# Kernel tuning notes

Measured on AMD Instinct MI355X. Metric: run time of the kernel, lower is better.

## Reference

```python
import jax, jax.numpy as jnp
import numpy as np

EPS = 1e-6
K = 20
B, N = 4, 4096
HID, CDIM = 128, 64


def vn_lin(W, x):
    # W: [Cout, Cin], x: [B, Cin, 3, ...] -> [B, Cout, 3, ...]
    return jnp.einsum('oc,bc...->bo...', W, x)


def vn_leaky(x, d, ns=0.0):
    # vector-neuron leaky ReLU: reflect the part of x anti-aligned with direction d
    dot = jnp.sum(x * d, axis=2, keepdims=True)
    dsq = jnp.sum(d * d, axis=2, keepdims=True)
    return ns * x + (1.0 - ns) * jnp.where(dot >= 0, x, x - (dot / (dsq + EPS)) * d)


def vn_max_pool(x, Wd):
    # pool over the LAST axis, picking per-(b,c) the vector maximizing <x, d>
    d = vn_lin(Wd, x)
    dot = jnp.sum(x * d, axis=2, keepdims=True)            # [B,C,1,...,L]
    idx = jnp.broadcast_to(jnp.argmax(dot, axis=-1), x.shape[:-1])
    return jnp.take_along_axis(x, idx[..., None], axis=-1)[..., 0]


def graph_feature_cross(pts, k):
    # pts: [B, N, 3] -> [B, 3ch, 3vec, N, k] with channels (nbr-x, x, cross(nbr,x))
    sq = jnp.sum(pts * pts, axis=-1)
    inner = jnp.einsum('bnd,bmd->bnm', pts, pts)
    neg_dist = 2.0 * inner - sq[:, :, None] - sq[:, None, :]
    _, idx = jax.lax.top_k(neg_dist, k)                     # [B, N, k]
    nbr = jax.vmap(lambda p, i: p[i])(pts, idx)             # [B, N, k, 3]
    x = jnp.broadcast_to(pts[:, :, None, :], nbr.shape)
    cross = jnp.cross(nbr, x, axis=-1)
    feat = jnp.stack([nbr - x, x, cross], axis=3)           # [B, N, k, 3ch, 3vec]
    return jnp.transpose(feat, (0, 3, 4, 1, 2))


def resblock(x, a0, f0, a1, f1, sc):
    net = vn_lin(f0, vn_leaky(x, vn_lin(a0, x)))
    dx = vn_lin(f1, vn_leaky(net, vn_lin(a1, net)))
    return vn_lin(sc, x) + dx


def _init(key, shape, fan_in):
    return jax.random.normal(key, shape, jnp.float32) / np.sqrt(fan_in)


def setup_inputs():
    key = jax.random.key(0)
    ks = jax.random.split(key, 14)
    return {
        'pc': jax.random.normal(ks[0], (B, N, 3), jnp.float32),
        'conv_Wf': _init(ks[1], (64, 3), 3),
        'conv_Wd': _init(ks[2], (64, 3), 3),
        'pool_pos_Wd': _init(ks[3], (64, 64), 64),
        'fc_pos_W': _init(ks[4], (2 * HID, 64), 64),
        'blk_a0': _init(ks[5], (5, 2 * HID, 2 * HID), 2 * HID),
        'blk_f0': _init(ks[6], (5, HID, 2 * HID), 2 * HID),
        'blk_a1': _init(ks[7], (5, HID, HID), HID),
        'blk_f1': _init(ks[8], (5, HID, HID), HID),
        'blk_sc': _init(ks[9], (5, HID, 2 * HID), 2 * HID),
        'pool_Wd': _init(ks[10], (5, HID, HID), HID),
        'actc_Wd': _init(ks[11], (HID, HID), HID),
        'fcc_W': _init(ks[12], (CDIM, HID), HID),
    }


def reference(pc, conv_Wf, conv_Wd, pool_pos_Wd, fc_pos_W, blk_a0, blk_f0, blk_a1, blk_f1, blk_sc, pool_Wd, actc_Wd, fcc_W):
    b = pc.shape[0]
    feat = graph_feature_cross(pc, K)                         # [B,3,3,N,k]
    net = vn_leaky(vn_lin(conv_Wf, feat), vn_lin(conv_Wd, feat))  # [B,64,3,N,k]
    net = vn_max_pool(net, pool_pos_Wd)                       # [B,64,3,N] (pool over k)
    net = vn_lin(fc_pos_W, net)                               # [B,256,3,N]
    for i in range(5):
        net = resblock(net, blk_a0[i], blk_f0[i], blk_a1[i], blk_f1[i], blk_sc[i])  # [B,128,3,N]
        if i < 4:
            pooled = vn_max_pool(net, pool_Wd[i])             # [B,128,3] (pool over N)
            net = jnp.concatenate([net, jnp.broadcast_to(pooled[..., None], net.shape)], axis=1)
    net = vn_max_pool(net, pool_Wd[4])                        # [B,128,3]
    c = vn_lin(fcc_W, vn_leaky(net, vn_lin(actc_Wd, net)))    # [B,64,3]
    return c.reshape(b, -1)                                   # [B,192]
```

## Files before the change

kernel.cpp:

```cpp
#include <hip/hip_runtime.h>
#include <hip/hip_bf16.h>
#include <math.h>

#define NPTS 4096
#define NB 4
#define KNN 20
#define NCOLS (3*NPTS)
#define NEG_INF (-__builtin_huge_valf())
#define DNEG_INF (-__builtin_huge_val())

typedef _Float16 f16x8 __attribute__((ext_vector_type(8)));
typedef _Float16 f16x4 __attribute__((ext_vector_type(4)));
typedef float f32x4 __attribute__((ext_vector_type(4)));

#define WOFF_FC 0
#define WOFF_A0 16384
#define WOFF_F0 344064
#define WOFF_A1 507904
#define WOFF_F1 589824
#define WOFF_SC 671744
#define WOFF_PW 835584
#define WTOT    917504

__global__ __launch_bounds__(512) void knn_kernel(const float* __restrict__ pc,
                                                  int* __restrict__ idx) {
  __shared__ float pts[NPTS*3];
  __shared__ double msv[2][8];
  __shared__ int    msn[2][8];
  int b = blockIdx.x >> 10;
  int rowblk = blockIdx.x & 1023;
  const float* pb = pc + (size_t)b*NPTS*3;
  for (int i = threadIdx.x; i < NPTS*3; i += 512) pts[i] = pb[i];
  __syncthreads();
  int wave = threadIdx.x >> 6;
  int lane = threadIdx.x & 63;
  int row  = wave >> 1;
  int half = wave & 1;
  int l128 = half*64 + lane;
  int n = rowblk*4 + row;
  double pn0 = pts[n*3+0], pn1 = pts[n*3+1], pn2 = pts[n*3+2];
  double sqn = pn0*pn0 + pn1*pn1 + pn2*pn2;
  double nd[32];
#pragma unroll
  for (int j = 0; j < 32; ++j) {
    int m = j*128 + l128;
    double q0 = pts[m*3+0], q1 = pts[m*3+1], q2 = pts[m*3+2];
    double inner = pn0*q0 + pn1*q1 + pn2*q2;
    double sqm = q0*q0 + q1*q1 + q2*q2;
    nd[j] = 2.0*inner - sqn - sqm;
  }
  double gm[2]; int gj[2];
#pragma unroll
  for (int g = 0; g < 2; ++g) {
    double v = nd[g*16]; int jb = g*16;
#pragma unroll
    for (int jj = 1; jj < 16; ++jj) {
      int j = g*16 + jj;
      bool take = nd[j] > v;
      v = take ? nd[j] : v;
      jb = take ? j : jb;
    }
    gm[g] = v; gj[g] = jb;
  }
  int* orow = idx + ((size_t)b*NPTS + n)*KNN;
  for (int t = 0; t < KNN; ++t) {
    double bv = gm[0]; int bj = gj[0];
    if (gm[1] > bv) { bv = gm[1]; bj = gj[1]; }
    int bm = bj*128 + l128;
#pragma unroll
    for (int s = 1; s < 64; s <<= 1) {
      double ov = __shfl_xor(bv, s, 64);
      int om = __shfl_xor(bm, s, 64);
      bool take = (ov > bv) || (ov == bv && om < bm);
      bv = take ? ov : bv;
      bm = take ? om : bm;
    }
    if (lane == 0) { msv[t&1][wave] = bv; msn[t&1][wave] = bm; }
    __syncthreads();
    {
      double pv = msv[t&1][wave^1]; int pm = msn[t&1][wave^1];
      bool take = (pv > bv) || (pv == bv && pm < bm);
      bv = take ? pv : bv;
      bm = take ? pm : bm;
    }
    if (half == 0 && lane == 0) orow[t] = bm;
    if (t < KNN-1) {
      int vic_l128 = bm & 127;
      int jw = bm >> 7;
      int vic_half = vic_l128 >> 6;
      if (vic_half == half) {
        bool iswl = (l128 == vic_l128);
        int gw = jw >> 4;
#define REBUILD(G) { \
  _Pragma("unroll") \
  for (int jj = 0; jj < 16; ++jj) { \
    int j = (G)*16 + jj; \
    if (iswl && j == jw) nd[j] = DNEG_INF; \
  } \
  double v = nd[(G)*16]; int jb = (G)*16; \
  _Pragma("unroll") \
  for (int jj = 1; jj < 16; ++jj) { \
    int j = (G)*16 + jj; \
    bool take = nd[j] > v; \
    v = take ? nd[j] : v; \
    jb = take ? j : jb; \
  } \
  gm[G] = v; gj[G] = jb; \
}
        if (gw == 0) REBUILD(0)
        else         REBUILD(1)
#undef REBUILD
      }
    }
  }
}

#define ECH 5
__global__ __launch_bounds__(128) void edgeconv_kernel(
    const float* __restrict__ pc, const int* __restrict__ knnidx,
    const float* __restrict__ Wf, const float* __restrict__ Wd,
    const float* __restrict__ Wp, float* __restrict__ outp) {
  __shared__ float xls[2*ECH*3*64];
  int wave = threadIdx.x >> 6, lane = threadIdx.x & 63;
  int pid0 = blockIdx.x * 2;
  int b = pid0 >> 12;
  int n = (pid0 & (NPTS-1)) + wave;
  const float* pb = pc + (size_t)b*NPTS*3;
  int c = lane;
  float wrow[64];
#pragma unroll
  for (int j = 0; j < 64; ++j) wrow[j] = Wp[c*64 + j];
  float wf0 = Wf[c*3+0], wf1 = Wf[c*3+1], wf2 = Wf[c*3+2];
  float wd0 = Wd[c*3+0], wd1 = Wd[c*3+1], wd2 = Wd[c*3+2];
  float f9[9];
#pragma unroll
  for (int i = 0; i < 9; ++i) f9[i] = 0.0f;
  if (lane < KNN) {
    int j = knnidx[((size_t)b*NPTS + n)*KNN + lane];
    float q0 = pb[j*3+0], q1 = pb[j*3+1], q2 = pb[j*3+2];
    float x0 = pb[n*3+0], x1 = pb[n*3+1], x2 = pb[n*3+2];
    f9[0] = q0-x0; f9[1] = q1-x1; f9[2] = q2-x2;
    f9[3] = x0;    f9[4] = x1;    f9[5] = x2;
    f9[6] = q1*x2 - q2*x1;
    f9[7] = q2*x0 - q0*x2;
    f9[8] = q0*x1 - q1*x0;
  }
  float* xw = &xls[wave*ECH*3*64];
  double bdot = DNEG_INF;
  float bx0 = 0.f, bx1 = 0.f, bx2 = 0.f;
  for (int k0 = 0; k0 < KNN; k0 += ECH) {
    for (int kc = 0; kc < ECH; ++kc) {
      int kk = k0 + kc;
      float fch[9];
#pragma unroll
      for (int i = 0; i < 9; ++i) fch[i] = __shfl(f9[i], kk, 64);
      float fv[3], dv[3];
#pragma unroll
      for (int v = 0; v < 3; ++v) {
        fv[v] = wf0*fch[v] + wf1*fch[3+v] + wf2*fch[6+v];
        dv[v] = wd0*fch[v] + wd1*fch[3+v] + wd2*fch[6+v];
      }
      float dot = fv[0]*dv[0] + fv[1]*dv[1] + fv[2]*dv[2];
      if (dot < 0.0f) {
        float dsq = dv[0]*dv[0] + dv[1]*dv[1] + dv[2]*dv[2];
        float s = dot / (dsq + 1e-6f);
        fv[0] -= s*dv[0]; fv[1] -= s*dv[1]; fv[2] -= s*dv[2];
      }
      xw[(0*ECH+kc)*64 + c] = fv[0];
      xw[(1*ECH+kc)*64 + c] = fv[1];
      xw[(2*ECH+kc)*64 + c] = fv[2];
    }
    for (int kc = 0; kc < ECH; ++kc) {
      float a0 = 0.f, a1 = 0.f, a2 = 0.f;
#pragma unroll
      for (int j = 0; j < 64; j += 4) {
        float4 v0 = *(const float4*)&xw[(0*ECH+kc)*64 + j];
        float4 v1 = *(const float4*)&xw[(1*ECH+kc)*64 + j];
        float4 v2 = *(const float4*)&xw[(2*ECH+kc)*64 + j];
        a0 += wrow[j]*v0.x + wrow[j+1]*v0.y + wrow[j+2]*v0.z + wrow[j+3]*v0.w;
        a1 += wrow[j]*v1.x + wrow[j+1]*v1.y + wrow[j+2]*v1.z + wrow[j+3]*v1.w;
        a2 += wrow[j]*v2.x + wrow[j+1]*v2.y + wrow[j+2]*v2.z + wrow[j+3]*v2.w;
      }
      float xc0 = xw[(0*ECH+kc)*64 + c];
      float xc1 = xw[(1*ECH+kc)*64 + c];
      float xc2 = xw[(2*ECH+kc)*64 + c];
      double dd = (double)xc0*a0 + (double)xc1*a1 + (double)xc2*a2;
      bool take = dd > bdot;
      bdot = take ? dd : bdot;
      bx0 = take ? xc0 : bx0;
      bx1 = take ? xc1 : bx1;
      bx2 = take ? xc2 : bx2;
    }
  }
  outp[((size_t)b*NCOLS + 0*NPTS + n)*64 + c] = bx0;
  outp[((size_t)b*NCOLS + 1*NPTS + n)*64 + c] = bx1;
  outp[((size_t)b*NCOLS + 2*NPTS + n)*64 + c] = bx2;
}

__global__ __launch_bounds__(256) void wsplit_kernel(
    const float* __restrict__ fc, const float* __restrict__ a0,
    const float* __restrict__ f0, const float* __restrict__ a1,
    const float* __restrict__ f1, const float* __restrict__ sc,
    const float* __restrict__ pw, _Float16* __restrict__ outp) {
  int i = blockIdx.x*256 + threadIdx.x;
  const float* src; int off;
  if      (i < WOFF_A0) { src = fc; off = WOFF_FC; }
  else if (i < WOFF_F0) { src = a0; off = WOFF_A0; }
  else if (i < WOFF_A1) { src = f0; off = WOFF_F0; }
  else if (i < WOFF_F1) { src = a1; off = WOFF_A1; }
  else if (i < WOFF_SC) { src = f1; off = WOFF_F1; }
  else if (i < WOFF_PW) { src = sc; off = WOFF_SC; }
  else                  { src = pw; off = WOFF_PW; }
  float w = src[i - off];
  _Float16 h = (_Float16)w;
  outp[i] = h;
  outp[i + WTOT] = (_Float16)(w - (float)h);
}

__global__ __launch_bounds__(256) void bias2_kernel(
    const float* __restrict__ Wa0, const float* __restrict__ Wsc,
    const float* __restrict__ pooled,
    float* __restrict__ biasA, float* __restrict__ biasS) {
  int id = blockIdx.x*256 + threadIdx.x;
  const float* W; float* dst; int Cout; int idx;
  if (id < NB*3*256) { W = Wa0; dst = biasA; Cout = 256; idx = id; }
  else               { W = Wsc; dst = biasS; Cout = 128; idx = id - NB*3*256; }
  int co = idx % Cout; int t = idx / Cout;
  int v = t % 3; int b = t / 3;
  double acc = 0.0;
  const float* wr = W + (size_t)co*256 + 128;
  const float* pp = pooled + (size_t)b*384 + v;
#pragma unroll 4
  for (int c = 0; c < 128; ++c)
    acc += (double)wr[c] * (double)pp[c*3];
  dst[idx] = (float)acc;
}

#define LDP 40
__global__ __launch_bounds__(256) void gemm_mfma(
    const _Float16* __restrict__ Wh, const _Float16* __restrict__ Wl,
    const float* __restrict__ X, const float* __restrict__ Z,
    const float* __restrict__ bias, float* __restrict__ Y,
    int Cin, int Wstride, int ldX, int ldY, int ldZ, int addZ, int Cbias) {
  __shared__ __align__(16) _Float16 Ah[64*LDP];
  __shared__ __align__(16) _Float16 Al[64*LDP];
  __shared__ __align__(16) _Float16 Bh[128*LDP];
  __shared__ __align__(16) _Float16 Bl[128*LDP];
  int b = blockIdx.z;
  int sp0 = blockIdx.x * 64;
  int co0 = blockIdx.y * 128;
  const float* Xb = X + ((size_t)b*NCOLS + sp0) * ldX;
  int t = threadIdx.x;
  int arow = t >> 2, akoff = (t & 3) * 8;
  int brow = t >> 1, bkoff = (t & 1) * 16;
  int wid = t >> 6, lane = t & 63;
  int wr = (wid >> 1) * 32, wc = (wid & 1) * 64;
  int lrow = lane & 15, lk = (lane >> 4) * 8;
  f32x4 acc[2][4];
#pragma unroll
  for (int f = 0; f < 2; ++f)
#pragma unroll
    for (int g = 0; g < 4; ++g)
#pragma unroll
      for (int r = 0; r < 4; ++r) acc[f][g][r] = 0.0f;

  for (int k0 = 0; k0 < Cin; k0 += 32) {
    const float* xs = Xb + (size_t)arow*ldX + k0 + akoff;
    float xv[8];
    *(float4*)&xv[0] = *(const float4*)&xs[0];
    *(float4*)&xv[4] = *(const float4*)&xs[4];
    _Float16 xh[8], xl[8];
#pragma unroll
    for (int j = 0; j < 8; ++j) {
      _Float16 h = (_Float16)xv[j];
      xh[j] = h; xl[j] = (_Float16)(xv[j] - (float)h);
    }
    *(f16x8*)&Ah[arow*LDP + akoff] = *(f16x8*)&xh[0];
    *(f16x8*)&Al[arow*LDP + akoff] = *(f16x8*)&xl[0];
    const _Float16* whs = Wh + (size_t)(co0 + brow)*Wstride + k0 + bkoff;
    const _Float16* wls = Wl + (size_t)(co0 + brow)*Wstride + k0 + bkoff;
    *(f16x8*)&Bh[brow*LDP + bkoff]     = *(const f16x8*)&whs[0];
    *(f16x8*)&Bh[brow*LDP + bkoff + 8] = *(const f16x8*)&whs[8];
    *(f16x8*)&Bl[brow*LDP + bkoff]     = *(const f16x8*)&wls[0];
    *(f16x8*)&Bl[brow*LDP + bkoff + 8] = *(const f16x8*)&wls[8];
    __syncthreads();
    f16x8 ah[2], al[2], bh[4], bl[4];
#pragma unroll
    for (int f = 0; f < 2; ++f) {
      ah[f] = *(f16x8*)&Ah[(wr + f*16 + lrow)*LDP + lk];
      al[f] = *(f16x8*)&Al[(wr + f*16 + lrow)*LDP + lk];
    }
#pragma unroll
    for (int g = 0; g < 4; ++g) {
      bh[g] = *(f16x8*)&Bh[(wc + g*16 + lrow)*LDP + lk];
      bl[g] = *(f16x8*)&Bl[(wc + g*16 + lrow)*LDP + lk];
    }
#pragma unroll
    for (int f = 0; f < 2; ++f)
#pragma unroll
      for (int g = 0; g < 4; ++g) {
        acc[f][g] = __builtin_amdgcn_mfma_f32_16x16x32_f16(ah[f], bh[g], acc[f][g], 0, 0, 0);
        acc[f][g] = __builtin_amdgcn_mfma_f32_16x16x32_f16(ah[f], bl[g], acc[f][g], 0, 0, 0);
        acc[f][g] = __builtin_amdgcn_mfma_f32_16x16x32_f16(al[f], bh[g], acc[f][g], 0, 0, 0);
      }
    __syncthreads();
  }
  int lr0 = (lane >> 4) * 4, lc = lane & 15;
  float badd[4] = {0.f, 0.f, 0.f, 0.f};
  if (bias) {
    int v = sp0 >> 12;
    const float* brow2 = bias + ((size_t)b*3 + v)*Cbias;
#pragma unroll
    for (int g = 0; g < 4; ++g) badd[g] = brow2[co0 + wc + g*16 + lc];
  }
#pragma unroll
  for (int f = 0; f < 2; ++f)
#pragma unroll
    for (int g = 0; g < 4; ++g)
#pragma unroll
      for (int r = 0; r < 4; ++r) {
        int sp = sp0 + wr + f*16 + lr0 + r;
        int co = co0 + wc + g*16 + lc;
        float val = acc[f][g][r] + badd[g];
        if (addZ) val += Z[((size_t)b*NCOLS + sp)*ldZ + co];
        Y[((size_t)b*NCOLS + sp)*ldY + co] = val;
      }
}

__global__ __launch_bounds__(256) void gemm_dual(
    const _Float16* __restrict__ W1h, const _Float16* __restrict__ W1l,
    const _Float16* __restrict__ W2h, const _Float16* __restrict__ W2l,
    const float* __restrict__ X1, const float* __restrict__ X2s,
    const float* __restrict__ bias, float* __restrict__ Y,
    int K2, int ldY, int Cbias) {
  __shared__ __align__(16) _Float16 Ah[64*LDP];
  __shared__ __align__(16) _Float16 Al[64*LDP];
  __shared__ __align__(16) _Float16 Bh[128*LDP];
  __shared__ __align__(16) _Float16 Bl[128*LDP];
  int b = blockIdx.z;
  int sp0 = blockIdx.x * 64;
  int co0 = blockIdx.y * 128;
  int t = threadIdx.x;
  int arow = t >> 2, akoff = (t & 3) * 8;
  int brow = t >> 1, bkoff = (t & 1) * 16;
  int wid = t >> 6, lane = t & 63;
  int wr = (wid >> 1) * 32, wc = (wid & 1) * 64;
  int lrow = lane & 15, lk = (lane >> 4) * 8;
  f32x4 acc[2][4];
#pragma unroll
  for (int f = 0; f < 2; ++f)
#pragma unroll
    for (int g = 0; g < 4; ++g)
#pragma unroll
      for (int r = 0; r < 4; ++r) acc[f][g][r] = 0.0f;

  int Ktot = 128 + K2;
  for (int k0 = 0; k0 < Ktot; k0 += 32) {
    const float* xs;
    const _Float16 *whs, *wls;
    if (k0 < 128) {
      xs  = X1 + ((size_t)b*NCOLS + sp0 + arow)*128 + k0 + akoff;
      whs = W1h + (size_t)(co0 + brow)*128 + k0 + bkoff;
      wls = W1l + (size_t)(co0 + brow)*128 + k0 + bkoff;
    } else {
      xs  = X2s + ((size_t)b*NCOLS + sp0 + arow)*256 + (k0-128) + akoff;
      whs = W2h + (size_t)(co0 + brow)*256 + (k0-128) + bkoff;
      wls = W2l + (size_t)(co0 + brow)*256 + (k0-128) + bkoff;
    }
    float xv[8];
    *(float4*)&xv[0] = *(const float4*)&xs[0];
    *(float4*)&xv[4] = *(const float4*)&xs[4];
    _Float16 xh[8], xl[8];
#pragma unroll
    for (int j = 0; j < 8; ++j) {
      _Float16 h = (_Float16)xv[j];
      xh[j] = h; xl[j] = (_Float16)(xv[j] - (float)h);
    }
    *(f16x8*)&Ah[arow*LDP + akoff] = *(f16x8*)&xh[0];
    *(f16x8*)&Al[arow*LDP + akoff] = *(f16x8*)&xl[0];
    *(f16x8*)&Bh[brow*LDP + bkoff]     = *(const f16x8*)&whs[0];
    *(f16x8*)&Bh[brow*LDP + bkoff + 8] = *(const f16x8*)&whs[8];
    *(f16x8*)&Bl[brow*LDP + bkoff]     = *(const f16x8*)&wls[0];
    *(f16x8*)&Bl[brow*LDP + bkoff + 8] = *(const f16x8*)&wls[8];
    __syncthreads();
    f16x8 ah[2], al[2], bh[4], bl[4];
#pragma unroll
    for (int f = 0; f < 2; ++f) {
      ah[f] = *(f16x8*)&Ah[(wr + f*16 + lrow)*LDP + lk];
      al[f] = *(f16x8*)&Al[(wr + f*16 + lrow)*LDP + lk];
    }
#pragma unroll
    for (int g = 0; g < 4; ++g) {
      bh[g] = *(f16x8*)&Bh[(wc + g*16 + lrow)*LDP + lk];
      bl[g] = *(f16x8*)&Bl[(wc + g*16 + lrow)*LDP + lk];
    }
#pragma unroll
    for (int f = 0; f < 2; ++f)
#pragma unroll
      for (int g = 0; g < 4; ++g) {
        acc[f][g] = __builtin_amdgcn_mfma_f32_16x16x32_f16(ah[f], bh[g], acc[f][g], 0, 0, 0);
        acc[f][g] = __builtin_amdgcn_mfma_f32_16x16x32_f16(ah[f], bl[g], acc[f][g], 0, 0, 0);
        acc[f][g] = __builtin_amdgcn_mfma_f32_16x16x32_f16(al[f], bh[g], acc[f][g], 0, 0, 0);
      }
    __syncthreads();
  }
  int lr0 = (lane >> 4) * 4, lc = lane & 15;
  float badd[4] = {0.f, 0.f, 0.f, 0.f};
  if (bias) {
    int v = sp0 >> 12;
    const float* brow2 = bias + ((size_t)b*3 + v)*Cbias;
#pragma unroll
    for (int g = 0; g < 4; ++g) badd[g] = brow2[co0 + wc + g*16 + lc];
  }
#pragma unroll
  for (int f = 0; f < 2; ++f)
#pragma unroll
    for (int g = 0; g < 4; ++g)
#pragma unroll
      for (int r = 0; r < 4; ++r) {
        int sp = sp0 + wr + f*16 + lr0 + r;
        int co = co0 + wc + g*16 + lc;
        Y[((size_t)b*NCOLS + sp)*ldY + co] = acc[f][g][r] + badd[g];
      }
}

template<int FM>
__global__ __launch_bounds__(256) void gemm_leaky(
    const _Float16* __restrict__ Wh, const _Float16* __restrict__ Wl,
    const float* __restrict__ X, const float* __restrict__ pooled,
    const float* __restrict__ bias, float* __restrict__ Y,
    int Cin, int Wstride, int ldX, int ldY, int Cbias) {
  constexpr int BM = FM*32;
  __shared__ __align__(16) _Float16 Ah[BM*LDP];
  __shared__ __align__(16) _Float16 Al[BM*LDP];
  __shared__ __align__(16) _Float16 Bh[128*LDP];
  __shared__ __align__(16) _Float16 Bl[128*LDP];
  int b = blockIdx.z;
  int n0 = blockIdx.x * BM;
  int co0 = blockIdx.y * 128;
  int t = threadIdx.x;
  constexpr int APT = BM/8;
  constexpr int TPR = 32/APT;
  int arow = t / TPR, akoff = (t % TPR) * APT;
  int brow = t >> 1, bkoff = (t & 1) * 16;
  int wid = t >> 6, lane = t & 63;
  int wr = (wid >> 1) * (BM/2), wc = (wid & 1) * 64;
  int lrow = lane & 15, lk = (lane >> 4) * 8;
  f32x4 acc[3][FM][4];
#pragma unroll
  for (int v = 0; v < 3; ++v)
#pragma unroll
    for (int f = 0; f < FM; ++f)
#pragma unroll
      for (int g = 0; g < 4; ++g)
#pragma unroll
        for (int r = 0; r < 4; ++r) acc[v][f][g][r] = 0.0f;

  for (int v = 0; v < 3; ++v) {
    const float* Xb = X + ((size_t)b*NCOLS + (size_t)v*NPTS + n0) * ldX;
    for (int k0 = 0; k0 < Cin; k0 += 32) {
      const float* xs = Xb + (size_t)arow*ldX + k0 + akoff;
      float xv[APT];
#pragma unroll
      for (int j = 0; j < APT; j += 4)
        *(float4*)&xv[j] = *(const float4*)&xs[j];
      _Float16 xh[APT], xl[APT];
#pragma unroll
      for (int j = 0; j < APT; ++j) {
        _Float16 h = (_Float16)xv[j];
        xh[j] = h; xl[j] = (_Float16)(xv[j] - (float)h);
      }
      if (APT == 8) {
        *(f16x8*)&Ah[arow*LDP + akoff] = *(f16x8*)&xh[0];
        *(f16x8*)&Al[arow*LDP + akoff] = *(f16x8*)&xl[0];
      } else {
        *(f16x4*)&Ah[arow*LDP + akoff] = *(f16x4*)&xh[0];
        *(f16x4*)&Al[arow*LDP + akoff] = *(f16x4*)&xl[0];
      }
      const _Float16* whs = Wh + (size_t)(co0 + brow)*Wstride + k0 + bkoff;
      const _Float16* wls = Wl + (size_t)(co0 + brow)*Wstride + k0 + bkoff;
      *(f16x8*)&Bh[brow*LDP + bkoff]     = *(const f16x8*)&whs[0];
      *(f16x8*)&Bh[brow*LDP + bkoff + 8] = *(const f16x8*)&whs[8];
      *(f16x8*)&Bl[brow*LDP + bkoff]     = *(const f16x8*)&wls[0];
      *(f16x8*)&Bl[brow*LDP + bkoff + 8] = *(const f16x8*)&wls[8];
      __syncthreads();
      f16x8 ah[FM], al[FM], bh[4], bl[4];
#pragma unroll
      for (int f = 0; f < FM; ++f) {
        ah[f] = *(f16x8*)&Ah[(wr + f*16 + lrow)*LDP + lk];
        al[f] = *(f16x8*)&Al[(wr + f*16 + lrow)*LDP + lk];
      }
#pragma unroll
      for (int g = 0; g < 4; ++g) {
        bh[g] = *(f16x8*)&Bh[(wc + g*16 + lrow)*LDP + lk];
        bl[g] = *(f16x8*)&Bl[(wc + g*16 + lrow)*LDP + lk];
      }
#pragma unroll
      for (int f = 0; f < FM; ++f)
#pragma unroll
        for (int g = 0; g < 4; ++g) {
          acc[v][f][g] = __builtin_amdgcn_mfma_f32_16x16x32_f16(ah[f], bh[g], acc[v][f][g], 0, 0, 0);
          acc[v][f][g] = __builtin_amdgcn_mfma_f32_16x16x32_f16(ah[f], bl[g], acc[v][f][g], 0, 0, 0);
          acc[v][f][g] = __builtin_amdgcn_mfma_f32_16x16x32_f16(al[f], bh[g], acc[v][f][g], 0, 0, 0);
        }
      __syncthreads();
    }
  }
  int lr0 = (lane >> 4) * 4, lc = lane & 15;
  float badd[3][4];
#pragma unroll
  for (int v = 0; v < 3; ++v)
#pragma unroll
    for (int g = 0; g < 4; ++g) {
      badd[v][g] = bias ? bias[((size_t)b*3 + v)*Cbias + co0 + wc + g*16 + lc] : 0.0f;
    }
  bool xfromX = (pooled == nullptr) || (co0 < 128);
#pragma unroll
  for (int f = 0; f < FM; ++f)
#pragma unroll
    for (int g = 0; g < 4; ++g)
#pragma unroll
      for (int r = 0; r < 4; ++r) {
        int n = n0 + wr + f*16 + lr0 + r;
        int co = co0 + wc + g*16 + lc;
        float x0, x1, x2;
        if (xfromX) {
          x0 = X[((size_t)b*NCOLS + 0*NPTS + n)*ldX + co];
          x1 = X[((size_t)b*NCOLS + 1*NPTS + n)*ldX + co];
          x2 = X[((size_t)b*NCOLS + 2*NPTS + n)*ldX + co];
        } else {
          const float* pp = pooled + (size_t)b*384 + (co - 128)*3;
          x0 = pp[0]; x1 = pp[1]; x2 = pp[2];
        }
        float d0 = acc[0][f][g][r] + badd[0][g];
        float d1 = acc[1][f][g][r] + badd[1][g];
        float d2 = acc[2][f][g][r] + badd[2][g];
        float dot = x0*d0 + x1*d1 + x2*d2;
        float u0 = x0, u1 = x1, u2 = x2;
        if (dot < 0.0f) {
          float dsq = d0*d0 + d1*d1 + d2*d2;
          float s = dot / (dsq + 1e-6f);
          u0 = x0 - s*d0; u1 = x1 - s*d1; u2 = x2 - s*d2;
        }
        Y[((size_t)b*NCOLS + 0*NPTS + n)*ldY + co] = u0;
        Y[((size_t)b*NCOLS + 1*NPTS + n)*ldY + co] = u1;
        Y[((size_t)b*NCOLS + 2*NPTS + n)*ldY + co] = u2;
      }
}

__global__ __launch_bounds__(256) void gemm_pool(
    const _Float16* __restrict__ Wh, const _Float16* __restrict__ Wl,
    const float* __restrict__ X,
    double* __restrict__ pv, int* __restrict__ pn) {
  __shared__ __align__(16) _Float16 Ah[64*LDP];
  __shared__ __align__(16) _Float16 Al[64*LDP];
  __shared__ __align__(16) _Float16 Bh[128*LDP];
  __shared__ __align__(16) _Float16 Bl[128*LDP];
  int b = blockIdx.z;
  int n0 = blockIdx.x * 64;
  int t = threadIdx.x;
  int arow = t >> 2, akoff = (t & 3) * 8;
  int brow = t >> 1, bkoff = (t & 1) * 16;
  int wid = t >> 6, lane = t & 63;
  int wr = (wid >> 1) * 32, wc = (wid & 1) * 64;
  int lrow = lane & 15, lk = (lane >> 4) * 8;
  f32x4 acc[3][2][4];
#pragma unroll
  for (int v = 0; v < 3; ++v)
#pragma unroll
    for (int f = 0; f < 2; ++f)
#pragma unroll
      for (int g = 0; g < 4; ++g)
#pragma unroll
        for (int r = 0; r < 4; ++r) acc[v][f][g][r] = 0.0f;

  for (int v = 0; v < 3; ++v) {
    const float* Xb = X + ((size_t)b*NCOLS + (size_t)v*NPTS + n0) * 256;
    for (int k0 = 0; k0 < 128; k0 += 32) {
      const float* xs = Xb + (size_t)arow*256 + k0 + akoff;
      float xv[8];
      *(float4*)&xv[0] = *(const float4*)&xs[0];
      *(float4*)&xv[4] = *(const float4*)&xs[4];
      _Float16 xh[8], xl[8];
#pragma unroll
      for (int j = 0; j < 8; ++j) {
        _Float16 h = (_Float16)xv[j];
        xh[j] = h; xl[j] = (_Float16)(xv[j] - (float)h);
      }
      *(f16x8*)&Ah[arow*LDP + akoff] = *(f16x8*)&xh[0];
      *(f16x8*)&Al[arow*LDP + akoff] = *(f16x8*)&xl[0];
      const _Float16* whs = Wh + (size_t)brow*128 + k0 + bkoff;
      const _Float16* wls = Wl + (size_t)brow*128 + k0 + bkoff;
      *(f16x8*)&Bh[brow*LDP + bkoff]     = *(const f16x8*)&whs[0];
      *(f16x8*)&Bh[brow*LDP + bkoff + 8] = *(const f16x8*)&whs[8];
      *(f16x8*)&Bl[brow*LDP + bkoff]     = *(const f16x8*)&wls[0];
      *(f16x8*)&Bl[brow*LDP + bkoff + 8] = *(const f16x8*)&wls[8];
      __syncthreads();
      f16x8 ah[2], al[2], bh[4], bl[4];
#pragma unroll
      for (int f = 0; f < 2; ++f) {
        ah[f] = *(f16x8*)&Ah[(wr + f*16 + lrow)*LDP + lk];
        al[f] = *(f16x8*)&Al[(wr + f*16 + lrow)*LDP + lk];
      }
#pragma unroll
      for (int g = 0; g < 4; ++g) {
        bh[g] = *(f16x8*)&Bh[(wc + g*16 + lrow)*LDP + lk];
        bl[g] = *(f16x8*)&Bl[(wc + g*16 + lrow)*LDP + lk];
      }
#pragma unroll
      for (int f = 0; f < 2; ++f)
#pragma unroll
        for (int g = 0; g < 4; ++g) {
          acc[v][f][g] = __builtin_amdgcn_mfma_f32_16x16x32_f16(ah[f], bh[g], acc[v][f][g], 0, 0, 0);
          acc[v][f][g] = __builtin_amdgcn_mfma_f32_16x16x32_f16(ah[f], bl[g], acc[v][f][g], 0, 0, 0);
          acc[v][f][g] = __builtin_amdgcn_mfma_f32_16x16x32_f16(al[f], bh[g], acc[v][f][g], 0, 0, 0);
        }
      __syncthreads();
    }
  }
  int lr0 = (lane >> 4) * 4, lc = lane & 15;
  double bestv[4]; int bestn[4];
#pragma unroll
  for (int g = 0; g < 4; ++g) { bestv[g] = DNEG_INF; bestn[g] = 0x7fffffff; }
#pragma unroll
  for (int f = 0; f < 2; ++f)
#pragma unroll
    for (int r = 0; r < 4; ++r) {
      int n = n0 + wr + f*16 + lr0 + r;
#pragma unroll
      for (int g = 0; g < 4; ++g) {
        int co = wc + g*16 + lc;
        double dot =
            (double)X[((size_t)b*NCOLS + 0*NPTS + n)*256 + co] * (double)acc[0][f][g][r]
          + (double)X[((size_t)b*NCOLS + 1*NPTS + n)*256 + co] * (double)acc[1][f][g][r]
          + (double)X[((size_t)b*NCOLS + 2*NPTS + n)*256 + co] * (double)acc[2][f][g][r];
        bool take = (dot > bestv[g]) || (dot == bestv[g] && n < bestn[g]);
        bestv[g] = take ? dot : bestv[g];
        bestn[g] = take ? n : bestn[g];
      }
    }
#pragma unroll
  for (int s = 16; s < 64; s <<= 1) {
#pragma unroll
    for (int g = 0; g < 4; ++g) {
      double ov = __shfl_xor(bestv[g], s, 64);
      int on = __shfl_xor(bestn[g], s, 64);
      bool take = (ov > bestv[g]) || (ov == bestv[g] && on < bestn[g]);
      bestv[g] = take ? ov : bestv[g];
      bestn[g] = take ? on : bestn[g];
    }
  }
  double* cdv = (double*)Ah;
  int*    cdn = (int*)Bh;
  if (lane < 16) {
#pragma unroll
    for (int g = 0; g < 4; ++g) {
      cdv[(wid*4 + g)*16 + lane] = bestv[g];
      cdn[(wid*4 + g)*16 + lane] = bestn[g];
    }
  }
  __syncthreads();
  if (t < 128) {
    int c = t;
    int wq = c >> 6;
    int g = (c >> 4) & 3, l2 = c & 15;
    double v0 = cdv[((wq)*4 + g)*16 + l2];   int n0v = cdn[((wq)*4 + g)*16 + l2];
    double v1 = cdv[((wq+2)*4 + g)*16 + l2]; int n1v = cdn[((wq+2)*4 + g)*16 + l2];
    bool take = (v1 > v0) || (v1 == v0 && n1v < n0v);
    double bv = take ? v1 : v0;
    int bn = take ? n1v : n0v;
    pv[((size_t)b*64 + blockIdx.x)*128 + c] = bv;
    pn[((size_t)b*64 + blockIdx.x)*128 + c] = bn;
  }
}

__global__ __launch_bounds__(128) void pool2_kernel(
    const double* __restrict__ pv, const int* __restrict__ pn,
    const float* __restrict__ Net, float* __restrict__ pooled, int ldN) {
  int b = blockIdx.x, c = threadIdx.x;
  double bv = DNEG_INF; int bn = 0x7fffffff;
  for (int ch = 0; ch < 64; ++ch) {
    double v = pv[((size_t)b*64 + ch)*128 + c];
    int nn = pn[((size_t)b*64 + ch)*128 + c];
    if (v > bv || (v == bv && nn < bn)) { bv = v; bn = nn; }
  }
#pragma unroll
  for (int v = 0; v < 3; ++v)
    pooled[(size_t)b*384 + c*3 + v] = Net[((size_t)b*NCOLS + v*NPTS + bn)*ldN + c];
}

__global__ __launch_bounds__(128) void head_kernel(
    const float* __restrict__ pooled, const float* __restrict__ Wa,
    const float* __restrict__ Wc, float* __restrict__ out) {
  __shared__ float xp[128*3], up[128*3];
  int b = blockIdx.x, c = threadIdx.x;
#pragma unroll
  for (int v = 0; v < 3; ++v) xp[c*3+v] = pooled[(size_t)b*384 + c*3 + v];
  __syncthreads();
  float a0 = 0.f, a1 = 0.f, a2 = 0.f;
  for (int j = 0; j < 128; ++j) {
    float w = Wa[c*128+j];
    a0 += w*xp[j*3+0]; a1 += w*xp[j*3+1]; a2 += w*xp[j*3+2];
  }
  float x0 = xp[c*3+0], x1 = xp[c*3+1], x2 = xp[c*3+2];
  float dot = x0*a0 + x1*a1 + x2*a2;
  float u0 = x0, u1 = x1, u2 = x2;
  if (dot < 0.0f) {
    float dsq = a0*a0 + a1*a1 + a2*a2;
    float s = dot / (dsq + 1e-6f);
    u0 = x0 - s*a0; u1 = x1 - s*a1; u2 = x2 - s*a2;
  }
  up[c*3+0] = u0; up[c*3+1] = u1; up[c*3+2] = u2;
  __syncthreads();
  if (c < 64) {
    float o0 = 0.f, o1 = 0.f, o2 = 0.f;
    for (int j = 0; j < 128; ++j) {
      float w = Wc[c*128+j];
      o0 += w*up[j*3+0]; o1 += w*up[j*3+1]; o2 += w*up[j*3+2];
    }
    out[(size_t)b*192 + c*3 + 0] = o0;
    out[(size_t)b*192 + c*3 + 1] = o1;
    out[(size_t)b*192 + c*3 + 2] = o2;
  }
}

extern "C" void kernel_launch(void* const* d_in, const int* in_sizes, int n_in,
                              void* d_out, int out_size, void* d_ws, size_t ws_size,
                              hipStream_t stream) {
  const float* pc    = (const float*)d_in[0];
  const float* cWf   = (const float*)d_in[1];
  const float* cWd   = (const float*)d_in[2];
  const float* pposW = (const float*)d_in[3];
  const float* fcW   = (const float*)d_in[4];
  const float* ba0   = (const float*)d_in[5];
  const float* bf0   = (const float*)d_in[6];
  const float* ba1   = (const float*)d_in[7];
  const float* bf1   = (const float*)d_in[8];
  const float* bscW  = (const float*)d_in[9];
  const float* pWd   = (const float*)d_in[10];
  const float* aWd   = (const float*)d_in[11];
  const float* fccW  = (const float*)d_in[12];
  float* out = (float*)d_out;
  char* ws = (char*)d_ws;
  const size_t MB = 1u << 20;
  const size_t KB = 1u << 10;
  int*      idxb   = (int*)(ws);
  float*    X1     = (float*)(ws + 2*MB);
  float*    X2     = (float*)(ws + 52*MB);
  float*    conv   = (float*)(ws + 52*MB);
  float*    T      = (float*)(ws + 102*MB);
  float*    T2     = T;
  float*    Hn     = (float*)(ws + 152*MB);
  float*    pooled = (float*)(ws + 178*MB);
  double*   pv     = (double*)(ws + 178*MB + 16*KB);
  int*      pn     = (int*)(ws + 178*MB + 288*KB);
  float*    biasA  = (float*)(ws + 178*MB + 448*KB);
  float*    biasS  = (float*)(ws + 178*MB + 512*KB);
  _Float16* Wsp    = (_Float16*)(ws + 179*MB);
  _Float16* WspLo  = Wsp + WTOT;

  wsplit_kernel<<<WTOT/256, 256, 0, stream>>>(fcW, ba0, bf0, ba1, bf1, bscW, pWd, Wsp);
  knn_kernel<<<NB*NPTS/4, 512, 0, stream>>>(pc, idxb);
  edgeconv_kernel<<<NB*NPTS/2, 128, 0, stream>>>(pc, idxb, cWf, cWd, pposW, conv);
  gemm_mfma<<<dim3(192, 2, NB), 256, 0, stream>>>(Wsp + WOFF_FC, WspLo + WOFF_FC,
      conv, nullptr, nullptr, X1, 64, 64, 64, 256, 0, 0, 0);

  float* Xin = X1; float* Xout = X2;
  for (int i = 0; i < 5; ++i) {
    const _Float16* a0h = Wsp   + WOFF_A0 + (size_t)i*65536;
    const _Float16* a0l = WspLo + WOFF_A0 + (size_t)i*65536;
    const _Float16* f0h = Wsp   + WOFF_F0 + (size_t)i*32768;
    const _Float16* f0l = WspLo + WOFF_F0 + (size_t)i*32768;
    const _Float16* f1h = Wsp   + WOFF_F1 + (size_t)i*16384;
    const _Float16* f1l = WspLo + WOFF_F1 + (size_t)i*16384;
    const _Float16* a1h = Wsp   + WOFF_A1 + (size_t)i*16384;
    const _Float16* a1l = WspLo + WOFF_A1 + (size_t)i*16384;
    const _Float16* sch = Wsp   + WOFF_SC + (size_t)i*32768;
    const _Float16* scl = WspLo + WOFF_SC + (size_t)i*32768;
    const _Float16* pwh = Wsp   + WOFF_PW + (size_t)i*16384;
    const _Float16* pwl = WspLo + WOFF_PW + (size_t)i*16384;
    int KA = (i == 0) ? 256 : 128;
    const float* bA = (i == 0) ? nullptr : biasA;
    const float* bS = (i == 0) ? nullptr : biasS;
    const float* lp = (i == 0) ? nullptr : pooled;
    if (i > 0) {
      bias2_kernel<<<(NB*3*384+255)/256,256,0,stream>>>(
          ba0 + (size_t)i*65536, bscW + (size_t)i*32768, pooled, biasA, biasS);
    }
    gemm_leaky<2><<<dim3(NPTS/64, 2, NB), 256, 0, stream>>>(a0h, a0l, Xin, lp, bA, T,
        KA, 256, 256, 256, 256);
    gemm_mfma<<<dim3(192,1,NB),256,0,stream>>>(f0h, f0l, T, nullptr, nullptr, Hn,
        256, 256, 256, 128, 0, 0, 0);
    gemm_leaky<1><<<dim3(NPTS/32, 1, NB), 256, 0, stream>>>(a1h, a1l, Hn, nullptr, nullptr, T2,
        128, 128, 128, 128, 0);
    gemm_dual<<<dim3(192,1,NB),256,0,stream>>>(f1h, f1l, sch, scl, T2, Xin, bS, Xout,
        KA, 256, 128);
    gemm_pool<<<dim3(NPTS/64,1,NB),256,0,stream>>>(pwh, pwl, Xout, pv, pn);
    pool2_kernel<<<NB,128,0,stream>>>(pv, pn, Xout, pooled, 256);
    if (i < 4) { float* tmp = Xin; Xin = Xout; Xout = tmp; }
  }
  head_kernel<<<NB,128,0,stream>>>(pooled, aWd, fccW, out);
}
```

Baseline: 1.310 ms.

## Halve edgeconv weight registers via LDS and fuse bias kernel into pool2

The edgeconv kernel now keeps only half of each thread's 64-entry Wp row in registers and reads the other half from a transposed shared-memory copy. This lowers register pressure, which may allow more waves to be resident. Separately, the per-iteration bias2 kernel is removed: its work is folded into the pool2 kernel, which computes the next iteration's biases from the pooled vectors held in shared memory. That saves four launches but runs the bias math on only 4 blocks of 128 threads, so that stage has far less parallelism than before.

```diff
diff --git a/kernel.cpp b/kernel.cpp
--- a/kernel.cpp
+++ b/kernel.cpp
@@ -121,15 +121,20 @@
     const float* __restrict__ Wf, const float* __restrict__ Wd,
     const float* __restrict__ Wp, float* __restrict__ outp) {
   __shared__ float xls[2*ECH*3*64];
+  __shared__ float wpT[32*64];
   int wave = threadIdx.x >> 6, lane = threadIdx.x & 63;
   int pid0 = blockIdx.x * 2;
   int b = pid0 >> 12;
   int n = (pid0 & (NPTS-1)) + wave;
   const float* pb = pc + (size_t)b*NPTS*3;
   int c = lane;
-  float wrow[64];
-#pragma unroll
-  for (int j = 0; j < 64; ++j) wrow[j] = Wp[c*64 + j];
+  for (int idx = threadIdx.x; idx < 32*64; idx += 128) {
+    int jj = idx >> 6, cc = idx & 63;
+    wpT[jj*64 + cc] = Wp[cc*64 + 32 + jj];
+  }
+  float wrow[32];
+#pragma unroll
+  for (int j = 0; j < 32; ++j) wrow[j] = Wp[c*64 + j];
   float wf0 = Wf[c*3+0], wf1 = Wf[c*3+1], wf2 = Wf[c*3+2];
   float wd0 = Wd[c*3+0], wd1 = Wd[c*3+1], wd2 = Wd[c*3+2];
   float f9[9];
@@ -145,6 +150,7 @@
     f9[7] = q2*x0 - q0*x2;
     f9[8] = q0*x1 - q1*x0;
   }
+  __syncthreads();
   float* xw = &xls[wave*ECH*3*64];
   double bdot = DNEG_INF;
   float bx0 = 0.f, bx1 = 0.f, bx2 = 0.f;
@@ -173,13 +179,26 @@
     for (int kc = 0; kc < ECH; ++kc) {
       float a0 = 0.f, a1 = 0.f, a2 = 0.f;
 #pragma unroll
-      for (int j = 0; j < 64; j += 4) {
+      for (int j = 0; j < 32; j += 4) {
         float4 v0 = *(const float4*)&xw[(0*ECH+kc)*64 + j];
         float4 v1 = *(const float4*)&xw[(1*ECH+kc)*64 + j];
         float4 v2 = *(const float4*)&xw[(2*ECH+kc)*64 + j];
         a0 += wrow[j]*v0.x + wrow[j+1]*v0.y + wrow[j+2]*v0.z + wrow[j+3]*v0.w;
         a1 += wrow[j]*v1.x + wrow[j+1]*v1.y + wrow[j+2]*v1.z + wrow[j+3]*v1.w;
         a2 += wrow[j]*v2.x + wrow[j+1]*v2.y + wrow[j+2]*v2.z + wrow[j+3]*v2.w;
+      }
+#pragma unroll
+      for (int j = 32; j < 64; j += 4) {
+        float4 v0 = *(const float4*)&xw[(0*ECH+kc)*64 + j];
+        float4 v1 = *(const float4*)&xw[(1*ECH+kc)*64 + j];
+        float4 v2 = *(const float4*)&xw[(2*ECH+kc)*64 + j];
+        float w0 = wpT[(j-32)*64 + c];
+        float w1 = wpT[(j-31)*64 + c];
+        float w2 = wpT[(j-30)*64 + c];
+        float w3 = wpT[(j-29)*64 + c];
+        a0 += w0*v0.x + w1*v0.y + w2*v0.z + w3*v0.w;
+        a1 += w0*v1.x + w1*v1.y + w2*v1.z + w3*v1.w;
+        a2 += w0*v2.x + w1*v2.y + w2*v2.z + w3*v2.w;
       }
       float xc0 = xw[(0*ECH+kc)*64 + c];
       float xc1 = xw[(1*ECH+kc)*64 + c];
@@ -215,25 +234,6 @@
   _Float16 h = (_Float16)w;
   outp[i] = h;
   outp[i + WTOT] = (_Float16)(w - (float)h);
-}
-
-__global__ __launch_bounds__(256) void bias2_kernel(
-    const float* __restrict__ Wa0, const float* __restrict__ Wsc,
-    const float* __restrict__ pooled,
-    float* __restrict__ biasA, float* __restrict__ biasS) {
-  int id = blockIdx.x*256 + threadIdx.x;
-  const float* W; float* dst; int Cout; int idx;
-  if (id < NB*3*256) { W = Wa0; dst = biasA; Cout = 256; idx = id; }
-  else               { W = Wsc; dst = biasS; Cout = 128; idx = id - NB*3*256; }
-  int co = idx % Cout; int t = idx / Cout;
-  int v = t % 3; int b = t / 3;
-  double acc = 0.0;
-  const float* wr = W + (size_t)co*256 + 128;
-  const float* pp = pooled + (size_t)b*384 + v;
-#pragma unroll 4
-  for (int c = 0; c < 128; ++c)
-    acc += (double)wr[c] * (double)pp[c*3];
-  dst[idx] = (float)acc;
 }
 
 #define LDP 40
@@ -674,9 +674,12 @@
   }
 }
 
-__global__ __launch_bounds__(128) void pool2_kernel(
+__global__ __launch_bounds__(128) void pool2bias_kernel(
     const double* __restrict__ pv, const int* __restrict__ pn,
-    const float* __restrict__ Net, float* __restrict__ pooled, int ldN) {
+    const float* __restrict__ Net, float* __restrict__ pooled,
+    const float* __restrict__ Wa0, const float* __restrict__ Wsc,
+    float* __restrict__ biasA, float* __restrict__ biasS, int lastIter) {
+  __shared__ float pl[384];
   int b = blockIdx.x, c = threadIdx.x;
   double bv = DNEG_INF; int bn = 0x7fffffff;
   for (int ch = 0; ch < 64; ++ch) {
@@ -685,8 +688,31 @@
     if (v > bv || (v == bv && nn < bn)) { bv = v; bn = nn; }
   }
 #pragma unroll
-  for (int v = 0; v < 3; ++v)
-    pooled[(size_t)b*384 + c*3 + v] = Net[((size_t)b*NCOLS + v*NPTS + bn)*ldN + c];
+  for (int v = 0; v < 3; ++v) {
+    float val = Net[((size_t)b*NCOLS + v*NPTS + bn)*256 + c];
+    pooled[(size_t)b*384 + c*3 + v] = val;
+    pl[c*3 + v] = val;
+  }
+  if (lastIter) return;
+  __syncthreads();
+  for (int tt = c; tt < 1152; tt += 128) {
+    const float* wr; float* dst; int v;
+    if (tt < 768) {
+      v = tt >> 8; int co = tt & 255;
+      wr = Wa0 + (size_t)co*256 + 128;
+      dst = &biasA[((size_t)b*3 + v)*256 + co];
+    } else {
+      int u = tt - 768;
+      v = u >> 7; int co = u & 127;
+      wr = Wsc + (size_t)co*256 + 128;
+      dst = &biasS[((size_t)b*3 + v)*128 + co];
+    }
+    double acc = 0.0;
+#pragma unroll 4
+    for (int cc = 0; cc < 128; ++cc)
+      acc += (double)wr[cc] * (double)pl[cc*3 + v];
+    *dst = (float)acc;
+  }
 }
 
 __global__ __launch_bounds__(128) void head_kernel(
@@ -783,10 +809,6 @@
     const float* bA = (i == 0) ? nullptr : biasA;
     const float* bS = (i == 0) ? nullptr : biasS;
     const float* lp = (i == 0) ? nullptr : pooled;
-    if (i > 0) {
-      bias2_kernel<<<(NB*3*384+255)/256,256,0,stream>>>(
-          ba0 + (size_t)i*65536, bscW + (size_t)i*32768, pooled, biasA, biasS);
-    }
     gemm_leaky<2><<<dim3(NPTS/64, 2, NB), 256, 0, stream>>>(a0h, a0l, Xin, lp, bA, T,
         KA, 256, 256, 256, 256);
     gemm_mfma<<<dim3(192,1,NB),256,0,stream>>>(f0h, f0l, T, nullptr, nullptr, Hn,
@@ -796,7 +818,10 @@
     gemm_dual<<<dim3(192,1,NB),256,0,stream>>>(f1h, f1l, sch, scl, T2, Xin, bS, Xout,
         KA, 256, 128);
     gemm_pool<<<dim3(NPTS/64,1,NB),256,0,stream>>>(pwh, pwl, Xout, pv, pn);
-    pool2_kernel<<<NB,128,0,stream>>>(pv, pn, Xout, pooled, 256);
+    pool2bias_kernel<<<NB,128,0,stream>>>(pv, pn, Xout, pooled,
+        ba0 + (size_t)(i+1 < 5 ? i+1 : 0)*65536,
+        bscW + (size_t)(i+1 < 5 ? i+1 : 0)*32768,
+        biasA, biasS, (i == 4) ? 1 : 0);
     if (i < 4) { float* tmp = Xin; Xin = Xout; Xout = tmp; }
   }
   head_kernel<<<NB,128,0,stream>>>(pooled, aWd, fccW, out);
```

Result: slower. 1.447 ms (+10.5%).
